# Kernel optimization log

Hardware: AMD Instinct MI355X
Metric: run time of the kernel (lower is better)

Reference implementation:

```python
import jax, jax.numpy as jnp
import numpy as np

N = 200000      # nodes
E_EDGES = 600000
G = 8000        # graphs
F_IN = 16
EMB = 128
L = 5           # GIN layers
C = 12          # targets
BN_EPS = 1e-5


def _bn(x, s, b, m, v):
    # BatchNorm1d in eval mode: normalize with stored running stats
    return (x - m) * jax.lax.rsqrt(v + BN_EPS) * s + b


def _mlp(x, w1, b1, s1, bb1, m1, v1, w2, b2, s2, bb2, m2, v2):
    h = jax.nn.relu(_bn(x @ w1 + b1, s1, bb1, m1, v1))
    return jax.nn.relu(_bn(h @ w2 + b2, s2, bb2, m2, v2))


def setup_inputs() -> dict:
    key = jax.random.key(0)
    ks = iter(jax.random.split(key, 64))
    inp = {}
    def nrm(shape, fan):
        return (jax.random.normal(next(ks), shape, jnp.float32) / np.sqrt(fan)).astype(jnp.float32)
    def bn_set(name, shape):
        inp[name + '_scale'] = jax.random.uniform(next(ks), shape, jnp.float32) * 0.5 + 0.75
        inp[name + '_bias'] = jax.random.normal(next(ks), shape, jnp.float32) * 0.1
        inp[name + '_mean'] = jax.random.normal(next(ks), shape, jnp.float32) * 0.1
        inp[name + '_var'] = jax.random.uniform(next(ks), shape, jnp.float32) * 0.5 + 0.75

    inp['x'] = jax.random.normal(next(ks), (N, F_IN), jnp.float32)
    src = jax.random.randint(next(ks), (E_EDGES,), 0, N, jnp.int32)
    dst = jax.random.randint(next(ks), (E_EDGES,), 0, N, jnp.int32)
    inp['edge_index'] = jnp.stack([src, dst])
    # sorted batch ids; every graph gets at least one node (avoid empty segment_max)
    inp['batch'] = jnp.sort(jnp.concatenate([
        jnp.arange(G, dtype=jnp.int32),
        jax.random.randint(next(ks), (N - G,), 0, G, jnp.int32)]))

    inp['init_w1'] = nrm((F_IN, EMB), F_IN)
    inp['init_b1'] = jnp.zeros((EMB,), jnp.float32)
    bn_set('init_bn1', (EMB,))
    inp['init_w2'] = nrm((EMB, EMB), EMB)
    inp['init_b2'] = jnp.zeros((EMB,), jnp.float32)
    bn_set('init_bn2', (EMB,))
    inp['init_lin_w'] = nrm((EMB, C), EMB)
    inp['init_lin_b'] = jnp.zeros((C,), jnp.float32)
    inp['eps'] = jnp.zeros((L,), jnp.float32)  # train_eps init 0.0
    inp['lw1'] = nrm((L, EMB, EMB), EMB)
    inp['lb1'] = jnp.zeros((L, EMB), jnp.float32)
    bn_set('lbn1', (L, EMB))
    inp['lw2'] = nrm((L, EMB, EMB), EMB)
    inp['lb2'] = jnp.zeros((L, EMB), jnp.float32)
    bn_set('lbn2', (L, EMB))
    inp['llin_w'] = nrm((L, EMB, C), EMB)
    inp['llin_b'] = jnp.zeros((L, C), jnp.float32)
    return inp


def _forward(edge_index, batch, x, init_w1, init_b1, init_bn1_scale, init_bn1_bias,
             init_bn1_mean, init_bn1_var, init_w2, init_b2, init_bn2_scale,
             init_bn2_bias, init_bn2_mean, init_bn2_var, init_lin_w, init_lin_b,
             eps, lw1, lb1, lbn1_scale, lbn1_bias, lbn1_mean, lbn1_var,
             lw2, lb2, lbn2_scale, lbn2_bias, lbn2_mean, lbn2_var, llin_w, llin_b):
    src, dst = edge_index[0], edge_index[1]
    h = _mlp(x, init_w1, init_b1, init_bn1_scale, init_bn1_bias, init_bn1_mean,
             init_bn1_var, init_w2, init_b2, init_bn2_scale, init_bn2_bias,
             init_bn2_mean, init_bn2_var)  # [N, EMB]
    # initial readout: linear then global max pool over graphs
    out = jax.ops.segment_max(h @ init_lin_w + init_lin_b, batch, num_segments=G)  # [G, C]
    for l in range(L):
        # GINConv: h <- MLP((1+eps)*h + sum_{j in N(i)} h_j)
        agg = jax.ops.segment_sum(h[src], dst, num_segments=N)  # gather + scatter-add
        h = _mlp((1.0 + eps[l]) * h + agg,
                 lw1[l], lb1[l], lbn1_scale[l], lbn1_bias[l], lbn1_mean[l], lbn1_var[l],
                 lw2[l], lb2[l], lbn2_scale[l], lbn2_bias[l], lbn2_mean[l], lbn2_var[l])
        # per-layer readout: global max pool then linear
        out = out + jax.ops.segment_max(h, batch, num_segments=G) @ llin_w[l] + llin_b[l]
    return out


def reference(x, edge_index, batch, init_w1, init_b1, init_bn1_scale, init_bn1_bias,
              init_bn1_mean, init_bn1_var, init_w2, init_b2, init_bn2_scale,
              init_bn2_bias, init_bn2_mean, init_bn2_var, init_lin_w, init_lin_b,
              eps, lw1, lb1, lbn1_scale, lbn1_bias, lbn1_mean, lbn1_var,
              lw2, lb2, lbn2_scale, lbn2_bias, lbn2_mean, lbn2_var, llin_w, llin_b):
    return _forward(edge_index, batch, x, init_w1, init_b1, init_bn1_scale,
                    init_bn1_bias, init_bn1_mean, init_bn1_var, init_w2, init_b2,
                    init_bn2_scale, init_bn2_bias, init_bn2_mean, init_bn2_var,
                    init_lin_w, init_lin_b, eps, lw1, lb1, lbn1_scale, lbn1_bias,
                    lbn1_mean, lbn1_var, lw2, lb2, lbn2_scale, lbn2_bias,
                    lbn2_mean, lbn2_var, llin_w, llin_b)
```

## Files before the change

kernel.cpp:

```cpp
#include <hip/hip_runtime.h>
#include <hip/hip_bf16.h>
#include <math.h>

#define EMB 128
#define CDIM 12
#define FIN 16
#define NLAYER 5
#define BN_EPS 1e-5f

typedef __attribute__((ext_vector_type(8))) _Float16 f16x8;
typedef __attribute__((ext_vector_type(2))) __fp16 fp16v2;
typedef __attribute__((ext_vector_type(4))) float f32x4;
typedef unsigned short ushort_t;

union h2u { fp16v2 h; unsigned u; };
union hu  { _Float16 h; ushort_t u; };

__device__ __forceinline__ void fsplit2(float a, float b, unsigned& hi, unsigned& lo) {
    h2u H; H.h = __builtin_amdgcn_cvt_pkrtz(a, b);
    float r0 = a - (float)H.h.x;
    float r1 = b - (float)H.h.y;
    h2u L; L.h = __builtin_amdgcn_cvt_pkrtz(r0, r1);
    hi = H.u; lo = L.u;
}

__device__ __forceinline__ unsigned pkrn(float x, float y) {
    hu A; A.h = (_Float16)x;
    hu B; B.h = (_Float16)y;
    return (unsigned)A.u | ((unsigned)B.u << 16);
}

__device__ __forceinline__ void acc8(float* f, uint4 v) {
    h2u c0, c1, c2, c3;
    c0.u = v.x; c1.u = v.y; c2.u = v.z; c3.u = v.w;
    f[0] += (float)c0.h.x; f[1] += (float)c0.h.y;
    f[2] += (float)c1.h.x; f[3] += (float)c1.h.y;
    f[4] += (float)c2.h.x; f[5] += (float)c2.h.y;
    f[6] += (float)c3.h.x; f[7] += (float)c3.h.y;
}

__device__ __forceinline__ unsigned swz(int node, unsigned byteoff) {
    return (unsigned)(node * 256 + byteoff) ^ (((unsigned)node & 7u) << 4);
}


__global__ __launch_bounds__(256) void k_gstart(const int* __restrict__ batch,
                                                int* __restrict__ gs, int N, int G) {
    int i = blockIdx.x * 256 + threadIdx.x;
    if (i >= N) return;
    if (i == 0) gs[0] = 0;
    else { int b = batch[i]; if (b != batch[i - 1]) gs[b] = i; }
    if (i == N - 1) gs[G] = N;
}

__global__ __launch_bounds__(256) void k_zero_i32(int* __restrict__ p, int n) {
    int i = blockIdx.x * 256 + threadIdx.x;
    if (i < n) p[i] = 0;
}

__global__ __launch_bounds__(256) void k_hist(const int* __restrict__ dst, int* __restrict__ cnt, int E) {
    int e = blockIdx.x * 256 + threadIdx.x;
    if (e < E) atomicAdd(&cnt[dst[e]], 1);
}

__global__ __launch_bounds__(256) void k_scan1(const int* __restrict__ cnt, int* __restrict__ rs,
                                               int* __restrict__ partials, int N) {
    __shared__ int tsum[256];
    int t = threadIdx.x;
    int base = blockIdx.x * 1024 + t * 4;
    int c[4];
    #pragma unroll
    for (int j = 0; j < 4; j++) c[j] = (base + j < N) ? cnt[base + j] : 0;
    int s = c[0] + c[1] + c[2] + c[3];
    tsum[t] = s;
    __syncthreads();
    for (int off = 1; off < 256; off <<= 1) {
        int v = (t >= off) ? tsum[t - off] : 0;
        __syncthreads();
        tsum[t] += v;
        __syncthreads();
    }
    int run = tsum[t] - s;
    if (t == 255) partials[blockIdx.x] = tsum[255];
    #pragma unroll
    for (int j = 0; j < 4; j++) {
        if (base + j < N) rs[base + j] = run;
        run += c[j];
    }
}

__global__ __launch_bounds__(256) void k_scan2(int* __restrict__ partials, int NB) {
    __shared__ int tmp[256];
    int t = threadIdx.x;
    int v = (t < NB) ? partials[t] : 0;
    tmp[t] = v;
    __syncthreads();
    for (int off = 1; off < 256; off <<= 1) {
        int u = (t >= off) ? tmp[t - off] : 0;
        __syncthreads();
        tmp[t] += u;
        __syncthreads();
    }
    if (t < NB) partials[t] = tmp[t] - v;
}

__global__ __launch_bounds__(256) void k_scan3(int* __restrict__ rs, const int* __restrict__ partials,
                                               int* __restrict__ cur_off, int N, int E) {
    int t = threadIdx.x;
    int base = blockIdx.x * 1024 + t * 4;
    int add = partials[blockIdx.x];
    #pragma unroll
    for (int j = 0; j < 4; j++) {
        int i = base + j;
        if (i < N) { int v = rs[i] + add; rs[i] = v; cur_off[i] = v; }
    }
    if (blockIdx.x == 0 && t == 0) rs[N] = E;
}

__global__ __launch_bounds__(256) void k_fillslots(const int* __restrict__ src, const int* __restrict__ dst,
                                                   int* __restrict__ cur_off, int* __restrict__ csr_src, int E) {
    int e = blockIdx.x * 256 + threadIdx.x;
    if (e >= E) return;
    int d = dst[e];
    int pos = atomicAdd(&cur_off[d], 1);
    csr_src[pos] = src[e];
}


__global__ __launch_bounds__(256) void k_prep(
        const float* __restrict__ init_w1, const float* __restrict__ init_b1,
        const float* __restrict__ b1s, const float* __restrict__ b1b,
        const float* __restrict__ b1m, const float* __restrict__ b1v,
        const float* __restrict__ init_w2, const float* __restrict__ init_b2,
        const float* __restrict__ i_s, const float* __restrict__ i_b,
        const float* __restrict__ i_m, const float* __restrict__ i_v,
        const float* __restrict__ lw1, const float* __restrict__ lb1,
        const float* __restrict__ l1s, const float* __restrict__ l1b,
        const float* __restrict__ l1m, const float* __restrict__ l1v,
        const float* __restrict__ lw2, const float* __restrict__ lb2,
        const float* __restrict__ l2s, const float* __restrict__ l2b,
        const float* __restrict__ l2m, const float* __restrict__ l2v,
        const float* __restrict__ ilin_w, const float* __restrict__ ilin_b,
        ushort_t* __restrict__ WT, float* __restrict__ biasf,
        float* __restrict__ W1f, float* __restrict__ bias1f,
        ushort_t* __restrict__ WzT, float* __restrict__ biasz) {
    int j = blockIdx.x;
    int t = threadIdx.x;
    __shared__ float alpha[EMB];

    if (j == 12) {
        if (t < 16) biasz[t] = (t < CDIM) ? ilin_b[t] : 0.f;
        for (int i = t; i < 16 * EMB; i += 256) {
            int f = i >> 7, k = i & 127;
            float w = (f < CDIM) ? ilin_w[k * CDIM + f] : 0.f;
            hu x; x.h = (_Float16)w;
            WzT[i] = x.u;
        }
        return;
    }
    if (j == 11) {
        if (t < EMB) {
            float a = b1s[t] * rsqrtf(b1v[t] + BN_EPS);
            alpha[t] = a;
            bias1f[t] = init_b1[t] * a + (b1b[t] - b1m[t] * a);
        }
        __syncthreads();
        for (int i = t; i < FIN * EMB; i += 256) W1f[i] = init_w1[i] * alpha[i & 127];
        return;
    }

    const float *W, *lb, *s, *bb, *m, *v;
    if (j == 0)      { W = init_w2;            lb = init_b2;        s = i_s;           bb = i_b;           m = i_m;           v = i_v; }
    else if (j <= 5) { int l = j - 1; W = lw1 + l * 16384; lb = lb1 + l * 128; s = l1s + l * 128; bb = l1b + l * 128; m = l1m + l * 128; v = l1v + l * 128; }
    else             { int l = j - 6; W = lw2 + l * 16384; lb = lb2 + l * 128; s = l2s + l * 128; bb = l2b + l * 128; m = l2m + l * 128; v = l2v + l * 128; }
    if (t < EMB) {
        float a = s[t] * rsqrtf(v[t] + BN_EPS);
        alpha[t] = a;
        biasf[j * EMB + t] = lb[t] * a + (bb[t] - m[t] * a);
    }
    __syncthreads();
    for (int i = t; i < EMB * EMB; i += 256) {
        int k = i >> 7, f = i & 127;
        float w = W[i] * alpha[f];
        hu x; x.h = (_Float16)w;
        WT[j * 16384 + f * 128 + k] = x.u;
    }
}


template<int MODE>
__global__ __launch_bounds__(512, 4) void k_layer(
        const float* __restrict__ xin, const ushort_t* __restrict__ hin,
        ushort_t* __restrict__ hout, float* __restrict__ z,
        const ushort_t* __restrict__ W1T, const float* __restrict__ b1,
        const ushort_t* __restrict__ W2T, const float* __restrict__ b2,
        const ushort_t* __restrict__ WzT, const float* __restrict__ bz,
        const float* __restrict__ W1f, const float* __restrict__ b1f,
        const int* __restrict__ rs, const int* __restrict__ csr, const float* __restrict__ epsp,
        int ntiles, int N) {
    constexpr int NT = (MODE == 1) ? 32 : 16;
    __shared__ ushort_t Ah[NT * 128], Al[NT * 128], Bh_[NT * 128], Bl_[NT * 128];
    __shared__ float W1s[(MODE == 0) ? FIN * EMB : 1];

    const int t = threadIdx.x;
    const int w = t >> 6;
    const int lane = t & 63;
    const int col = lane & 15, kg = lane >> 4;

    if (MODE == 0) {
        for (int i = t; i < FIN * EMB; i += 512) W1s[i] = W1f[i];
        __syncthreads();
    }

    f16x8 w1f[4], w2f[4], wzf[4];
    #pragma unroll
    for (int s = 0; s < 4; s++) {
        int off = (w * 16 + col) * EMB + s * 32 + kg * 8;
        w1f[s] = *(const f16x8*)(W1T + off);
        if (MODE == 1) w2f[s] = *(const f16x8*)(W2T + off);
        if (MODE == 0) {
            int zoff = col * EMB + s * 32 + kg * 8;
            wzf[s] = *(const f16x8*)(WzT + zoff);
        }
    }
    float4 bv1 = *(const float4*)&b1[w * 16 + kg * 4];
    float4 bv2, bvz;
    if (MODE == 1) bv2 = *(const float4*)&b2[w * 16 + kg * 4];
    if (MODE == 0) bvz = *(const float4*)&bz[kg * 4];
    float se = (MODE == 1) ? (1.f + epsp[0]) : 0.f;

    for (int tile = blockIdx.x; tile < ntiles; tile += gridDim.x) {
        const int n0 = tile * NT;

        if (MODE == 1) {
            const int nl = t >> 4, q2 = t & 15;
            const int nc = min(n0 + nl, N - 1);
            const uint4* hp = (const uint4*)hin;
            uint4 sv = hp[(size_t)nc * 16 + q2];
            float a[8] = {0.f, 0.f, 0.f, 0.f, 0.f, 0.f, 0.f, 0.f};
            acc8(a, sv);
            #pragma unroll
            for (int i = 0; i < 8; i++) a[i] *= se;
            int p = rs[nc], pe = rs[nc + 1];
            for (; p + 4 <= pe; p += 4) {
                int i0 = csr[p], i1 = csr[p + 1], i2 = csr[p + 2], i3 = csr[p + 3];
                uint4 v0 = hp[(size_t)i0 * 16 + q2];
                uint4 v1 = hp[(size_t)i1 * 16 + q2];
                uint4 v2 = hp[(size_t)i2 * 16 + q2];
                uint4 v3 = hp[(size_t)i3 * 16 + q2];
                acc8(a, v0); acc8(a, v1); acc8(a, v2); acc8(a, v3);
            }
            for (; p < pe; ++p) {
                uint4 v = hp[(size_t)csr[p] * 16 + q2];
                acc8(a, v);
            }
            uint4 H, L;
            fsplit2(a[0], a[1], H.x, L.x);
            fsplit2(a[2], a[3], H.y, L.y);
            fsplit2(a[4], a[5], H.z, L.z);
            fsplit2(a[6], a[7], H.w, L.w);
            unsigned ad = swz(nl, (unsigned)q2 * 16);
            *(uint4*)((char*)Ah + ad) = H;
            *(uint4*)((char*)Al + ad) = L;
        } else {
            const int nl = t >> 5, q = t & 31;
            const int nc = min(n0 + nl, N - 1);
            float4 ba = *(const float4*)&b1f[q * 4];
            float a0 = ba.x, a1 = ba.y, a2 = ba.z, a3 = ba.w;
            const float* xp = xin + (size_t)nc * FIN;
            #pragma unroll
            for (int k = 0; k < FIN; k++) {
                float xk = xp[k];
                float4 wv = *(const float4*)&W1s[k * EMB + q * 4];
                a0 += xk * wv.x; a1 += xk * wv.y; a2 += xk * wv.z; a3 += xk * wv.w;
            }
            a0 = fmaxf(a0, 0.f); a1 = fmaxf(a1, 0.f); a2 = fmaxf(a2, 0.f); a3 = fmaxf(a3, 0.f);
            uint2 H, L;
            fsplit2(a0, a1, H.x, L.x);
            fsplit2(a2, a3, H.y, L.y);
            unsigned ad = swz(nl, (unsigned)q * 8);
            *(uint2*)((char*)Ah + ad) = H;
            *(uint2*)((char*)Al + ad) = L;
        }
        __syncthreads();

        {
            f32x4 aA0 = (f32x4){0.f, 0.f, 0.f, 0.f}, aB0 = aA0, aA1 = aA0, aB1 = aA0;
            #pragma unroll
            for (int s = 0; s < 4; s++) {
                unsigned bo = (unsigned)((s * 32 + kg * 8) * 2);
                f16x8 xh0 = *(const f16x8*)((const char*)Ah + swz(col, bo));
                f16x8 xl0 = *(const f16x8*)((const char*)Al + swz(col, bo));
                aA0 = __builtin_amdgcn_mfma_f32_16x16x32_f16(w1f[s], xh0, aA0, 0, 0, 0);
                aB0 = __builtin_amdgcn_mfma_f32_16x16x32_f16(w1f[s], xl0, aB0, 0, 0, 0);
                if (MODE == 1) {
                    f16x8 xh1 = *(const f16x8*)((const char*)Ah + swz(col + 16, bo));
                    f16x8 xl1 = *(const f16x8*)((const char*)Al + swz(col + 16, bo));
                    aA1 = __builtin_amdgcn_mfma_f32_16x16x32_f16(w1f[s], xh1, aA1, 0, 0, 0);
                    aB1 = __builtin_amdgcn_mfma_f32_16x16x32_f16(w1f[s], xl1, aB1, 0, 0, 0);
                }
            }
            #pragma unroll
            for (int sub = 0; sub < ((MODE == 1) ? 2 : 1); sub++) {
                f32x4 aa = sub ? aA1 : aA0, ab = sub ? aB1 : aB0;
                float y0 = fmaxf(aa[0] + ab[0] + bv1.x, 0.f);
                float y1 = fmaxf(aa[1] + ab[1] + bv1.y, 0.f);
                float y2 = fmaxf(aa[2] + ab[2] + bv1.z, 0.f);
                float y3 = fmaxf(aa[3] + ab[3] + bv1.w, 0.f);
                if (MODE == 0) {
                    int onode = n0 + col;
                    if (onode < N) {
                        uint2 P; P.x = pkrn(y0, y1); P.y = pkrn(y2, y3);
                        *(uint2*)&hout[(size_t)onode * EMB + w * 16 + kg * 4] = P;
                    }
                }
                uint2 H, L;
                fsplit2(y0, y1, H.x, L.x);
                fsplit2(y2, y3, H.y, L.y);
                unsigned ad = swz(col + sub * 16, (unsigned)(w * 32 + kg * 8));
                *(uint2*)((char*)Bh_ + ad) = H;
                *(uint2*)((char*)Bl_ + ad) = L;
            }
        }
        __syncthreads();

        if (MODE == 1) {
            f32x4 aA0 = (f32x4){0.f, 0.f, 0.f, 0.f}, aB0 = aA0, aA1 = aA0, aB1 = aA0;
            #pragma unroll
            for (int s = 0; s < 4; s++) {
                unsigned bo = (unsigned)((s * 32 + kg * 8) * 2);
                f16x8 xh0 = *(const f16x8*)((const char*)Bh_ + swz(col, bo));
                f16x8 xl0 = *(const f16x8*)((const char*)Bl_ + swz(col, bo));
                f16x8 xh1 = *(const f16x8*)((const char*)Bh_ + swz(col + 16, bo));
                f16x8 xl1 = *(const f16x8*)((const char*)Bl_ + swz(col + 16, bo));
                aA0 = __builtin_amdgcn_mfma_f32_16x16x32_f16(w2f[s], xh0, aA0, 0, 0, 0);
                aB0 = __builtin_amdgcn_mfma_f32_16x16x32_f16(w2f[s], xl0, aB0, 0, 0, 0);
                aA1 = __builtin_amdgcn_mfma_f32_16x16x32_f16(w2f[s], xh1, aA1, 0, 0, 0);
                aB1 = __builtin_amdgcn_mfma_f32_16x16x32_f16(w2f[s], xl1, aB1, 0, 0, 0);
            }
            #pragma unroll
            for (int sub = 0; sub < 2; sub++) {
                f32x4 aa = sub ? aA1 : aA0, ab = sub ? aB1 : aB0;
                int onode = n0 + col + sub * 16;
                if (onode < N) {
                    float o0 = fmaxf(aa[0] + ab[0] + bv2.x, 0.f);
                    float o1 = fmaxf(aa[1] + ab[1] + bv2.y, 0.f);
                    float o2 = fmaxf(aa[2] + ab[2] + bv2.z, 0.f);
                    float o3 = fmaxf(aa[3] + ab[3] + bv2.w, 0.f);
                    uint2 P; P.x = pkrn(o0, o1); P.y = pkrn(o2, o3);
                    *(uint2*)&hout[(size_t)onode * EMB + w * 16 + kg * 4] = P;
                }
            }
        } else if (w == 0) {
            f32x4 aA0 = (f32x4){0.f, 0.f, 0.f, 0.f}, aB0 = aA0;
            #pragma unroll
            for (int s = 0; s < 4; s++) {
                unsigned bo = (unsigned)((s * 32 + kg * 8) * 2);
                f16x8 xh = *(const f16x8*)((const char*)Bh_ + swz(col, bo));
                f16x8 xl = *(const f16x8*)((const char*)Bl_ + swz(col, bo));
                aA0 = __builtin_amdgcn_mfma_f32_16x16x32_f16(wzf[s], xh, aA0, 0, 0, 0);
                aB0 = __builtin_amdgcn_mfma_f32_16x16x32_f16(wzf[s], xl, aB0, 0, 0, 0);
            }
            int onode = n0 + col;
            if (onode < N && kg < 3) {
                float4 o;
                o.x = aA0[0] + aB0[0] + bvz.x;
                o.y = aA0[1] + aB0[1] + bvz.y;
                o.z = aA0[2] + aB0[2] + bvz.z;
                o.w = aA0[3] + aB0[3] + bvz.w;
                *(float4*)&z[(size_t)onode * CDIM + kg * 4] = o;
            }
        }
    }
}


__global__ __launch_bounds__(64) void k_zmax(const float* __restrict__ z, const int* __restrict__ gs,
        float* __restrict__ out, int G) {
    int g = blockIdx.x;
    int t = threadIdx.x;
    if (t >= CDIM) return;
    int s0 = gs[g], e0 = gs[g + 1];
    float m = -INFINITY;
    for (int n = s0; n < e0; n++) m = fmaxf(m, z[(size_t)n * CDIM + t]);
    out[g * CDIM + t] = m;
}

__global__ __launch_bounds__(128) void k_readout(const ushort_t* __restrict__ h,
        const int* __restrict__ gs, const float* __restrict__ W,
        const float* __restrict__ lb, float* __restrict__ out, int G) {
    int g = blockIdx.x;
    int t = threadIdx.x;
    int s0 = gs[g], e0 = gs[g + 1];
    float mval = -INFINITY;
    for (int n = s0; n < e0; n++) {
        hu c; c.u = h[(size_t)n * EMB + t];
        mval = fmaxf(mval, (float)c.h);
    }
    __shared__ float mv[EMB];
    mv[t] = mval;
    __syncthreads();
    if (t < CDIM) {
        float acc = 0.f;
        for (int k = 0; k < EMB; k++) acc += mv[k] * W[k * CDIM + t];
        out[g * CDIM + t] += acc + lb[t];
    }
}


extern "C" void kernel_launch(void* const* d_in, const int* in_sizes, int n_in,
                              void* d_out, int out_size, void* d_ws, size_t ws_size,
                              hipStream_t stream) {
    const float* x        = (const float*)d_in[0];
    const int*   ei       = (const int*)d_in[1];
    const int*   batch    = (const int*)d_in[2];
    const float* init_w1  = (const float*)d_in[3];
    const float* init_b1  = (const float*)d_in[4];
    const float* ibn1_s   = (const float*)d_in[5];
    const float* ibn1_b   = (const float*)d_in[6];
    const float* ibn1_m   = (const float*)d_in[7];
    const float* ibn1_v   = (const float*)d_in[8];
    const float* init_w2  = (const float*)d_in[9];
    const float* init_b2  = (const float*)d_in[10];
    const float* ibn2_s   = (const float*)d_in[11];
    const float* ibn2_b   = (const float*)d_in[12];
    const float* ibn2_m   = (const float*)d_in[13];
    const float* ibn2_v   = (const float*)d_in[14];
    const float* ilin_w   = (const float*)d_in[15];
    const float* ilin_b   = (const float*)d_in[16];
    const float* eps      = (const float*)d_in[17];
    const float* lw1      = (const float*)d_in[18];
    const float* lb1      = (const float*)d_in[19];
    const float* lbn1_s   = (const float*)d_in[20];
    const float* lbn1_b   = (const float*)d_in[21];
    const float* lbn1_m   = (const float*)d_in[22];
    const float* lbn1_v   = (const float*)d_in[23];
    const float* lw2      = (const float*)d_in[24];
    const float* lb2      = (const float*)d_in[25];
    const float* lbn2_s   = (const float*)d_in[26];
    const float* lbn2_b   = (const float*)d_in[27];
    const float* lbn2_m   = (const float*)d_in[28];
    const float* lbn2_v   = (const float*)d_in[29];
    const float* llin_w   = (const float*)d_in[30];
    const float* llin_b   = (const float*)d_in[31];

    const int N = in_sizes[0] / FIN;
    const int E = in_sizes[1] / 2;
    const int G = out_size / CDIM;
    const int* src = ei;
    const int* dst = ei + E;
    float* out = (float*)d_out;

    char* wp = (char*)d_ws;
    auto alloc = [&](size_t bytes) { char* p = wp; wp += (bytes + 255) & ~(size_t)255; return p; };
    ushort_t* WT    = (ushort_t*)alloc((size_t)11 * 16384 * 2);
    float*    biasf = (float*)alloc(11 * EMB * 4);
    float*    W1f   = (float*)alloc(FIN * EMB * 4);
    float*    bias1f= (float*)alloc(EMB * 4);
    ushort_t* WzT   = (ushort_t*)alloc(16 * EMB * 2);
    float*    biasz = (float*)alloc(16 * 4);
    int*      gs    = (int*)alloc((size_t)(G + 1) * 4);
    int*      rs    = (int*)alloc((size_t)(N + 1) * 4);
    int*      curoff= (int*)alloc((size_t)N * 4);
    int*      csr   = (int*)alloc((size_t)E * 4);
    int*      parts = (int*)alloc(256 * 4);
    float*    zbuf  = (float*)alloc((size_t)N * CDIM * 4);
    ushort_t* bufP  = (ushort_t*)alloc((size_t)N * EMB * 2);
    ushort_t* bufQ  = (ushort_t*)alloc((size_t)N * EMB * 2);
    int*      cnt   = csr;

    const int NB = (N + 1023) / 1024;
    const int ntiles16 = (N + 15) / 16;
    const int ntiles32 = (N + 31) / 32;
    const int GRID = 2084;

    k_zero_i32<<<(N + 255) / 256, 256, 0, stream>>>(cnt, N);
    k_hist<<<(E + 255) / 256, 256, 0, stream>>>(dst, cnt, E);
    k_scan1<<<NB, 256, 0, stream>>>(cnt, rs, parts, N);
    k_scan2<<<1, 256, 0, stream>>>(parts, NB);
    k_scan3<<<NB, 256, 0, stream>>>(rs, parts, curoff, N, E);
    k_fillslots<<<(E + 255) / 256, 256, 0, stream>>>(src, dst, curoff, csr, E);
    k_gstart<<<(N + 255) / 256, 256, 0, stream>>>(batch, gs, N, G);
    k_prep<<<13, 256, 0, stream>>>(init_w1, init_b1, ibn1_s, ibn1_b, ibn1_m, ibn1_v,
                                   init_w2, init_b2, ibn2_s, ibn2_b, ibn2_m, ibn2_v,
                                   lw1, lb1, lbn1_s, lbn1_b, lbn1_m, lbn1_v,
                                   lw2, lb2, lbn2_s, lbn2_b, lbn2_m, lbn2_v,
                                   ilin_w, ilin_b,
                                   WT, biasf, W1f, bias1f, WzT, biasz);

    k_layer<0><<<GRID, 512, 0, stream>>>(x, nullptr, bufQ, zbuf,
                                         WT, biasf,
                                         nullptr, nullptr,
                                         WzT, biasz,
                                         W1f, bias1f,
                                         nullptr, nullptr, nullptr, ntiles16, N);
    k_zmax<<<G, 64, 0, stream>>>(zbuf, gs, out, G);

    ushort_t* cur = bufQ;
    ushort_t* oth = bufP;
    for (int l = 0; l < NLAYER; l++) {
        k_layer<1><<<GRID, 512, 0, stream>>>(nullptr, cur, oth, nullptr,
                                             WT + (size_t)(1 + l) * 16384, biasf + (1 + l) * EMB,
                                             WT + (size_t)(6 + l) * 16384, biasf + (6 + l) * EMB,
                                             nullptr, nullptr,
                                             nullptr, nullptr,
                                             rs, csr, eps + l, ntiles32, N);
        k_readout<<<G, 128, 0, stream>>>(oth, gs, llin_w + l * EMB * CDIM, llin_b + l * CDIM, out, G);
        ushort_t* tmp = cur; cur = oth; oth = tmp;
    }
}
```

Measured before the change: 762.0 us.

## Fuse segment-max readout into GIN layer epilogue and pad CSR rows to four

Each GIN layer kernel now computes the per-graph max pool in its epilogue with a segmented shuffle scan and float atomicMax into a per-layer buffer. This removes the separate readout kernel that re-read every node's features. One combine kernel applies all five readout linears at the end, and the last layer no longer writes its hidden output. CSR rows are padded to multiples of four with a dummy zero node, so neighbor indices load as uint4 with no scalar tail loop. The cost is extra atomics, a zeroing pass for the max buffer, and a larger padded CSR. Using atomicMax on raw float bits is only correct because the values are non-negative after ReLU.

```diff
diff --git a/kernel.cpp b/kernel.cpp
--- a/kernel.cpp
+++ b/kernel.cpp
@@ -58,6 +58,23 @@
     if (i < n) p[i] = 0;
 }
 
+__global__ __launch_bounds__(256) void k_fill_i32(int* __restrict__ p, int val, int n) {
+    int i = blockIdx.x * 256 + threadIdx.x;
+    if (i < n) p[i] = val;
+}
+
+__global__ __launch_bounds__(256) void k_zero_f32(float* __restrict__ p, int n) {
+    int i = blockIdx.x * 256 + threadIdx.x;
+    if (i < n) p[i] = 0.f;
+}
+
+__global__ __launch_bounds__(128) void k_zero_dummy(ushort_t* __restrict__ a,
+                                                    ushort_t* __restrict__ b, int N) {
+    int i = threadIdx.x;
+    a[(size_t)N * EMB + i] = 0;
+    b[(size_t)N * EMB + i] = 0;
+}
+
 __global__ __launch_bounds__(256) void k_hist(const int* __restrict__ dst, int* __restrict__ cnt, int E) {
     int e = blockIdx.x * 256 + threadIdx.x;
     if (e < E) atomicAdd(&cnt[dst[e]], 1);
@@ -70,7 +87,7 @@
     int base = blockIdx.x * 1024 + t * 4;
     int c[4];
     #pragma unroll
-    for (int j = 0; j < 4; j++) c[j] = (base + j < N) ? cnt[base + j] : 0;
+    for (int j = 0; j < 4; j++) c[j] = (base + j < N) ? ((cnt[base + j] + 3) & ~3) : 0;
     int s = c[0] + c[1] + c[2] + c[3];
     tsum[t] = s;
     __syncthreads();
@@ -84,7 +101,7 @@
     if (t == 255) partials[blockIdx.x] = tsum[255];
     #pragma unroll
     for (int j = 0; j < 4; j++) {
-        if (base + j < N) rs[base + j] = run;
+        if (base + j <= N) rs[base + j] = run;
         run += c[j];
     }
 }
@@ -105,16 +122,19 @@
 }
 
 __global__ __launch_bounds__(256) void k_scan3(int* __restrict__ rs, const int* __restrict__ partials,
-                                               int* __restrict__ cur_off, int N, int E) {
+                                               int* __restrict__ cur_off, int N) {
     int t = threadIdx.x;
     int base = blockIdx.x * 1024 + t * 4;
     int add = partials[blockIdx.x];
     #pragma unroll
     for (int j = 0; j < 4; j++) {
         int i = base + j;
-        if (i < N) { int v = rs[i] + add; rs[i] = v; cur_off[i] = v; }
-    }
-    if (blockIdx.x == 0 && t == 0) rs[N] = E;
+        if (i <= N) {
+            int v = rs[i] + add;
+            rs[i] = v;
+            if (i < N) cur_off[i] = v;
+        }
+    }
 }
 
 __global__ __launch_bounds__(256) void k_fillslots(const int* __restrict__ src, const int* __restrict__ dst,
@@ -197,6 +217,7 @@
         const ushort_t* __restrict__ WzT, const float* __restrict__ bz,
         const float* __restrict__ W1f, const float* __restrict__ b1f,
         const int* __restrict__ rs, const int* __restrict__ csr, const float* __restrict__ epsp,
+        const int* __restrict__ batch, float* __restrict__ smax,
         int ntiles, int N) {
     constexpr int NT = (MODE == 1) ? 32 : 16;
     __shared__ ushort_t Ah[NT * 128], Al[NT * 128], Bh_[NT * 128], Bl_[NT * 128];
@@ -242,17 +263,13 @@
             #pragma unroll
             for (int i = 0; i < 8; i++) a[i] *= se;
             int p = rs[nc], pe = rs[nc + 1];
-            for (; p + 4 <= pe; p += 4) {
-                int i0 = csr[p], i1 = csr[p + 1], i2 = csr[p + 2], i3 = csr[p + 3];
-                uint4 v0 = hp[(size_t)i0 * 16 + q2];
-                uint4 v1 = hp[(size_t)i1 * 16 + q2];
-                uint4 v2 = hp[(size_t)i2 * 16 + q2];
-                uint4 v3 = hp[(size_t)i3 * 16 + q2];
+            for (; p < pe; p += 4) {
+                uint4 idx = *(const uint4*)&csr[p];
+                uint4 v0 = hp[(size_t)idx.x * 16 + q2];
+                uint4 v1 = hp[(size_t)idx.y * 16 + q2];
+                uint4 v2 = hp[(size_t)idx.z * 16 + q2];
+                uint4 v3 = hp[(size_t)idx.w * 16 + q2];
                 acc8(a, v0); acc8(a, v1); acc8(a, v2); acc8(a, v3);
-            }
-            for (; p < pe; ++p) {
-                uint4 v = hp[(size_t)csr[p] * 16 + q2];
-                acc8(a, v);
             }
             uint4 H, L;
             fsplit2(a[0], a[1], H.x, L.x);
@@ -342,13 +359,39 @@
             for (int sub = 0; sub < 2; sub++) {
                 f32x4 aa = sub ? aA1 : aA0, ab = sub ? aB1 : aB0;
                 int onode = n0 + col + sub * 16;
-                if (onode < N) {
-                    float o0 = fmaxf(aa[0] + ab[0] + bv2.x, 0.f);
-                    float o1 = fmaxf(aa[1] + ab[1] + bv2.y, 0.f);
-                    float o2 = fmaxf(aa[2] + ab[2] + bv2.z, 0.f);
-                    float o3 = fmaxf(aa[3] + ab[3] + bv2.w, 0.f);
+                float o0 = fmaxf(aa[0] + ab[0] + bv2.x, 0.f);
+                float o1 = fmaxf(aa[1] + ab[1] + bv2.y, 0.f);
+                float o2 = fmaxf(aa[2] + ab[2] + bv2.z, 0.f);
+                float o3 = fmaxf(aa[3] + ab[3] + bv2.w, 0.f);
+                if (hout && onode < N) {
                     uint2 P; P.x = pkrn(o0, o1); P.y = pkrn(o2, o3);
                     *(uint2*)&hout[(size_t)onode * EMB + w * 16 + kg * 4] = P;
+                }
+                bool valid = onode < N;
+                float v0 = valid ? o0 : 0.f, v1 = valid ? o1 : 0.f;
+                float v2 = valid ? o2 : 0.f, v3 = valid ? o3 : 0.f;
+                int g = batch[min(onode, N - 1)];
+                #pragma unroll
+                for (int off = 1; off < 16; off <<= 1) {
+                    float u0 = __shfl_up(v0, off, 16);
+                    float u1 = __shfl_up(v1, off, 16);
+                    float u2 = __shfl_up(v2, off, 16);
+                    float u3 = __shfl_up(v3, off, 16);
+                    int gg = __shfl_up(g, off, 16);
+                    bool take = (col >= off) && (gg == g);
+                    if (take) {
+                        v0 = fmaxf(v0, u0); v1 = fmaxf(v1, u1);
+                        v2 = fmaxf(v2, u2); v3 = fmaxf(v3, u3);
+                    }
+                }
+                int gn = __shfl_down(g, 1, 16);
+                bool tail = (col == 15) || (gn != g);
+                if (tail) {
+                    unsigned* sp = (unsigned*)&smax[(size_t)g * EMB + w * 16 + kg * 4];
+                    atomicMax(sp + 0, __float_as_uint(v0));
+                    atomicMax(sp + 1, __float_as_uint(v1));
+                    atomicMax(sp + 2, __float_as_uint(v2));
+                    atomicMax(sp + 3, __float_as_uint(v3));
                 }
             }
         } else if (w == 0) {
@@ -386,24 +429,39 @@
     out[g * CDIM + t] = m;
 }
 
-__global__ __launch_bounds__(128) void k_readout(const ushort_t* __restrict__ h,
-        const int* __restrict__ gs, const float* __restrict__ W,
-        const float* __restrict__ lb, float* __restrict__ out, int G) {
+__global__ __launch_bounds__(128) void k_comb(const float* __restrict__ smax,
+        const float* __restrict__ llin_w, const float* __restrict__ llin_b,
+        float* __restrict__ out, int G) {
     int g = blockIdx.x;
     int t = threadIdx.x;
-    int s0 = gs[g], e0 = gs[g + 1];
-    float mval = -INFINITY;
-    for (int n = s0; n < e0; n++) {
-        hu c; c.u = h[(size_t)n * EMB + t];
-        mval = fmaxf(mval, (float)c.h);
-    }
-    __shared__ float mv[EMB];
-    mv[t] = mval;
+    __shared__ float mv[NLAYER][EMB];
+    #pragma unroll
+    for (int l = 0; l < NLAYER; l++)
+        mv[l][t] = smax[((size_t)l * G + g) * EMB + t];
+    __syncthreads();
+    __shared__ float parts_[8][16];
+    int c = t & 15, half = t >> 4;
+    float acc = 0.f;
+    if (c < CDIM) {
+        #pragma unroll
+        for (int l = 0; l < NLAYER; l++) {
+            const float* Wl = llin_w + l * EMB * CDIM;
+            #pragma unroll
+            for (int kk = 0; kk < 16; kk++) {
+                int k = half * 16 + kk;
+                acc += mv[l][k] * Wl[k * CDIM + c];
+            }
+        }
+    }
+    parts_[half][c] = acc;
     __syncthreads();
     if (t < CDIM) {
-        float acc = 0.f;
-        for (int k = 0; k < EMB; k++) acc += mv[k] * W[k * CDIM + t];
-        out[g * CDIM + t] += acc + lb[t];
+        float s = 0.f;
+        #pragma unroll
+        for (int hh = 0; hh < 8; hh++) s += parts_[hh][t];
+        #pragma unroll
+        for (int l = 0; l < NLAYER; l++) s += llin_b[l * CDIM + t];
+        out[g * CDIM + t] += s;
     }
 }
 
@@ -451,6 +509,8 @@
     const int* dst = ei + E;
     float* out = (float*)d_out;
 
+    const int EPADMAX = E + 3 * N;
+
     char* wp = (char*)d_ws;
     auto alloc = [&](size_t bytes) { char* p = wp; wp += (bytes + 255) & ~(size_t)255; return p; };
     ushort_t* WT    = (ushort_t*)alloc((size_t)11 * 16384 * 2);
@@ -462,23 +522,28 @@
     int*      gs    = (int*)alloc((size_t)(G + 1) * 4);
     int*      rs    = (int*)alloc((size_t)(N + 1) * 4);
     int*      curoff= (int*)alloc((size_t)N * 4);
-    int*      csr   = (int*)alloc((size_t)E * 4);
+    int*      csr   = (int*)alloc((size_t)EPADMAX * 4);
     int*      parts = (int*)alloc(256 * 4);
     float*    zbuf  = (float*)alloc((size_t)N * CDIM * 4);
-    ushort_t* bufP  = (ushort_t*)alloc((size_t)N * EMB * 2);
-    ushort_t* bufQ  = (ushort_t*)alloc((size_t)N * EMB * 2);
+    float*    smax  = (float*)alloc((size_t)NLAYER * G * EMB * 4);
+    ushort_t* bufP  = (ushort_t*)alloc((size_t)(N + 1) * EMB * 2);
+    ushort_t* bufQ  = (ushort_t*)alloc((size_t)(N + 1) * EMB * 2);
     int*      cnt   = csr;
 
-    const int NB = (N + 1023) / 1024;
+    const int NB = (N + 1 + 1023) / 1024;
     const int ntiles16 = (N + 15) / 16;
     const int ntiles32 = (N + 31) / 32;
     const int GRID = 2084;
+
+    k_zero_f32<<<((NLAYER * G * EMB) + 255) / 256, 256, 0, stream>>>(smax, NLAYER * G * EMB);
+    k_zero_dummy<<<1, 128, 0, stream>>>(bufP, bufQ, N);
 
     k_zero_i32<<<(N + 255) / 256, 256, 0, stream>>>(cnt, N);
     k_hist<<<(E + 255) / 256, 256, 0, stream>>>(dst, cnt, E);
     k_scan1<<<NB, 256, 0, stream>>>(cnt, rs, parts, N);
     k_scan2<<<1, 256, 0, stream>>>(parts, NB);
-    k_scan3<<<NB, 256, 0, stream>>>(rs, parts, curoff, N, E);
+    k_scan3<<<NB, 256, 0, stream>>>(rs, parts, curoff, N);
+    k_fill_i32<<<(EPADMAX + 255) / 256, 256, 0, stream>>>(csr, N, EPADMAX);
     k_fillslots<<<(E + 255) / 256, 256, 0, stream>>>(src, dst, curoff, csr, E);
     k_gstart<<<(N + 255) / 256, 256, 0, stream>>>(batch, gs, N, G);
     k_prep<<<13, 256, 0, stream>>>(init_w1, init_b1, ibn1_s, ibn1_b, ibn1_m, ibn1_v,
@@ -493,19 +558,22 @@
                                          nullptr, nullptr,
                                          WzT, biasz,
                                          W1f, bias1f,
-                                         nullptr, nullptr, nullptr, ntiles16, N);
+                                         nullptr, nullptr, nullptr,
+                                         nullptr, nullptr, ntiles16, N);
     k_zmax<<<G, 64, 0, stream>>>(zbuf, gs, out, G);
 
     ushort_t* cur = bufQ;
     ushort_t* oth = bufP;
     for (int l = 0; l < NLAYER; l++) {
-        k_layer<1><<<GRID, 512, 0, stream>>>(nullptr, cur, oth, nullptr,
+        ushort_t* houtl = (l == NLAYER - 1) ? nullptr : oth;
+        k_layer<1><<<GRID, 512, 0, stream>>>(nullptr, cur, houtl, nullptr,
                                              WT + (size_t)(1 + l) * 16384, biasf + (1 + l) * EMB,
                                              WT + (size_t)(6 + l) * 16384, biasf + (6 + l) * EMB,
                                              nullptr, nullptr,
                                              nullptr, nullptr,
-                                             rs, csr, eps + l, ntiles32, N);
-        k_readout<<<G, 128, 0, stream>>>(oth, gs, llin_w + l * EMB * CDIM, llin_b + l * CDIM, out, G);
+                                             rs, csr, eps + l,
+                                             batch, smax + (size_t)l * G * EMB, ntiles32, N);
         ushort_t* tmp = cur; cur = oth; oth = tmp;
     }
-}
+    k_comb<<<G, 128, 0, stream>>>(smax, llin_w, llin_b, out, G);
+}
```

Result: faster. 711.9 us (-6.6%).
